# Optimization experiments

Measured on AMD Instinct MI355X. Metric: run time of the kernel, lower is better.

## Reference

```python
import jax, jax.numpy as jnp
import numpy as np

B, L, CIN, C = 256, 65, 2053, 512
SCALE = 1.0 / float(np.sqrt(C))


def _attn_layer(x, Wq, bq, Wk, bk, Wv, bv):
    # x: [B, Cin, L]; Conv1d(kernel=1) == channel-mixing matmul
    q = jnp.einsum('oi,bil->bol', Wq, x) + bq[:, None]
    k = jnp.einsum('oi,bil->bol', Wk, x) + bk[:, None]
    v = jax.nn.leaky_relu(jnp.einsum('oi,bil->bol', Wv, x) + bv[:, None], 0.01)
    # att[b,l,m] = <q[:,l], k[:,m]> / sqrt(C); softmax over m
    att = jax.nn.softmax(jnp.einsum('bcl,bcm->blm', q, k) * SCALE, axis=-1)
    # original: sum_m att[b,l,1,m] * v[b,1,c,m] -> [B,L,C] -> permute -> [B,C,L]
    out = jnp.einsum('blm,bcm->bcl', att, v)
    return out + x if out.shape == x.shape else out  # residual only when channels match


def _transform(x, Wq0, bq0, Wk0, bk0, Wv0, bv0, Wq, bq, Wk, bk, Wv, bv):
    x = _attn_layer(x, Wq0, bq0, Wk0, bk0, Wv0, bv0)
    for n in range(3):  # layers 1..3, C->C with residual
        x = _attn_layer(x, Wq[n], bq[n], Wk[n], bk[n], Wv[n], bv[n])
    return x


def setup_inputs():
    key = jax.random.key(0)
    ks = jax.random.split(key, 20)
    s = 0.02
    inp = {
        'dataleft': jax.random.normal(ks[0], (B, L, CIN), jnp.float32),
        'dataright': jax.random.normal(ks[1], (B, L, CIN), jnp.float32),
        # layer-0 QKV conv1d (k=1) weights: [C, CIN]
        'Wq0': jax.random.normal(ks[2], (C, CIN), jnp.float32) * s,
        'bq0': jnp.zeros((C,), jnp.float32),
        'Wk0': jax.random.normal(ks[3], (C, CIN), jnp.float32) * s,
        'bk0': jnp.zeros((C,), jnp.float32),
        'Wv0': jax.random.normal(ks[4], (C, CIN), jnp.float32) * s,
        'bv0': jnp.zeros((C,), jnp.float32),
        # layers 1..3 stacked: [3, C, C]
        'Wq': jax.random.normal(ks[5], (3, C, C), jnp.float32) * s,
        'bq': jnp.zeros((3, C), jnp.float32),
        'Wk': jax.random.normal(ks[6], (3, C, C), jnp.float32) * s,
        'bk': jnp.zeros((3, C), jnp.float32),
        'Wv': jax.random.normal(ks[7], (3, C, C), jnp.float32) * s,
        'bv': jnp.zeros((3, C), jnp.float32),
        # classifier: fc1(1024->256), fc2(256->2)
        'W1': jax.random.normal(ks[8], (256, 2 * C), jnp.float32) * s,
        'b1': jnp.zeros((256,), jnp.float32),
        'W2': jax.random.normal(ks[9], (2, 256), jnp.float32) * s,
        'b2': jnp.zeros((2,), jnp.float32),
    }
    return inp


def reference(dataleft, dataright, Wq0, bq0, Wk0, bk0, Wv0, bv0,
              Wq, bq, Wk, bk, Wv, bv, W1, b1, W2, b2):
    xl = jnp.transpose(dataleft, (0, 2, 1))   # [B, CIN, L]
    xr = jnp.transpose(dataright, (0, 2, 1))
    xl = _transform(xl, Wq0, bq0, Wk0, bk0, Wv0, bv0, Wq, bq, Wk, bk, Wv, bv)
    xr = _transform(xr, Wq0, bq0, Wk0, bk0, Wv0, bv0, Wq, bq, Wk, bk, Wv, bv)
    # AdaptiveAvgPool2d((512,1)) on [B,512,L]: identity over channel dim, mean over L
    xl = jnp.mean(xl, axis=-1)  # [B, C]
    xr = jnp.mean(xr, axis=-1)
    h = jnp.concatenate([xl, xr], axis=1)            # [B, 2C]
    h = jax.nn.relu(h @ W1.T + b1)                   # [B, 256]
    y = h @ W2.T + b2                                # [B, 2]
    return y  # training mode: no final softmax
```

## Files before the change

### kernel.cpp

```cpp
#include <hip/hip_runtime.h>
#include <hip/hip_bf16.h>

#define BF16 __hip_bfloat16

typedef __bf16 bf16x8 __attribute__((ext_vector_type(8)));
typedef float f32x4 __attribute__((ext_vector_type(4)));

__device__ __forceinline__ void async_copy16(const void* g, void* l) {
    __builtin_amdgcn_global_load_lds(
        (const __attribute__((address_space(1))) void*)g,
        (__attribute__((address_space(3))) void*)l,
        16, 0, 0);
}

__global__ __launch_bounds__(256) void convert_pad_k(
    const float* __restrict__ src, BF16* __restrict__ dst,
    int Ks, int Kd) {
    const long r = blockIdx.y;
    const int k = (blockIdx.x * 256 + threadIdx.x) * 2;
    if (k >= Kd) return;
    float a = (k < Ks) ? src[r * Ks + k] : 0.f;
    float b = (k + 1 < Ks) ? src[r * Ks + k + 1] : 0.f;
    dst[r * Kd + k] = __float2bfloat16(a);
    dst[r * Kd + k + 1] = __float2bfloat16(b);
}

__global__ __launch_bounds__(512, 2) void gemm_qkv(
    const BF16* __restrict__ Xg, const BF16* __restrict__ Wg,
    const float* __restrict__ bqp, const float* __restrict__ bkp, const float* __restrict__ bvp,
    BF16* __restrict__ Qo, BF16* __restrict__ Ko, BF16* __restrict__ Vo,
    int K) {
    __shared__ __align__(16) BF16 As[3][256 * 64];
    __shared__ __align__(16) BF16 Bs[3][128 * 64];
    const int tid = threadIdx.x;
    const int w = tid >> 6;
    const int lane = tid & 63;
    const int quad = lane >> 4;
    const int l15 = lane & 15;
    const int linear = blockIdx.x + 12 * blockIdx.y;
    const int cpx = (12 * (int)gridDim.y) >> 3;
    const int id2 = (linear & 7) * cpx + (linear >> 3);
    const int bx = id2 % 12;
    const int by = id2 / 12;
    const long n0 = (long)by * 256;
    const long m0full = (long)bx * 128;
    const int sel = bx >> 2;
    const int mbase = (bx & 3) * 128;
    const int wr = (w >> 1) * 64;
    const int wc = (w & 1) * 64;
    const int KT = K >> 6;
    const int rl = lane >> 3;
    const int gsw = ((lane & 7) ^ (rl & 7)) * 8;
    const int rw = w * 8 + rl;

#define STAGE_TILE(k0, buf)                                                              \
    do {                                                                                 \
        _Pragma("unroll")                                                                \
        for (int r_ = 0; r_ < 4; ++r_)                                                   \
            async_copy16(Xg + (n0 + r_ * 64 + rw) * K + (k0) + gsw,                      \
                         &As[buf][(r_ * 64 + w * 8) * 64]);                              \
        _Pragma("unroll")                                                                \
        for (int r_ = 0; r_ < 2; ++r_)                                                   \
            async_copy16(Wg + (m0full + r_ * 64 + rw) * K + (k0) + gsw,                  \
                         &Bs[buf][(r_ * 64 + w * 8) * 64]);                              \
    } while (0)

    f32x4 acc[4][4] = {};
    STAGE_TILE(0, 0);
    STAGE_TILE(64, 1);
    int cb = 0;
    for (int kt = 0; kt < KT; ++kt) {
        if (kt + 1 < KT) {
            asm volatile("s_waitcnt vmcnt(6)\n\ts_barrier" ::: "memory");
        } else {
            asm volatile("s_waitcnt vmcnt(0)\n\ts_barrier" ::: "memory");
        }
        __builtin_amdgcn_sched_barrier(0);
        bf16x8 af[2][4], bfr[2][4];
#pragma unroll
        for (int s = 0; s < 2; ++s) {
#pragma unroll
            for (int i = 0; i < 4; ++i) {
                const int row = wr + i * 16 + l15;
                const int gx = ((s * 4 + quad) ^ (row & 7)) * 8;
                af[s][i] = *(const bf16x8*)&As[cb][row * 64 + gx];
            }
#pragma unroll
            for (int j = 0; j < 4; ++j) {
                const int row = wc + j * 16 + l15;
                const int gx = ((s * 4 + quad) ^ (row & 7)) * 8;
                bfr[s][j] = *(const bf16x8*)&Bs[cb][row * 64 + gx];
            }
        }
        if (kt + 2 < KT) {
            int nb = cb + 2;
            if (nb >= 3) nb -= 3;
            STAGE_TILE((kt + 2) << 6, nb);
        }
        __builtin_amdgcn_s_setprio(1);
#pragma unroll
        for (int s = 0; s < 2; ++s)
#pragma unroll
            for (int i = 0; i < 4; ++i)
#pragma unroll
                for (int j = 0; j < 4; ++j)
                    acc[i][j] = __builtin_amdgcn_mfma_f32_16x16x32_bf16(af[s][i], bfr[s][j], acc[i][j], 0, 0, 0);
        __builtin_amdgcn_s_setprio(0);
        ++cb;
        if (cb >= 3) cb -= 3;
    }
#undef STAGE_TILE

    const float* bp = (sel == 0) ? bqp : (sel == 1) ? bkp : bvp;
    BF16* out = (sel == 0) ? Qo : (sel == 1) ? Ko : Vo;
#pragma unroll
    for (int j = 0; j < 4; ++j) {
        const int m = mbase + wc + j * 16 + l15;
        const float bz = bp[m];
#pragma unroll
        for (int i = 0; i < 4; ++i) {
#pragma unroll
            for (int r = 0; r < 4; ++r) {
                const long n = n0 + wr + i * 16 + quad * 4 + r;
                float v = acc[i][j][r] + bz;
                if (sel == 2) v = (v >= 0.f) ? v : 0.01f * v;
                out[n * 512 + m] = __float2bfloat16(v);
            }
        }
    }
}

__global__ __launch_bounds__(256) void vtrans_k(const ushort* __restrict__ Vb,
                                                ushort* __restrict__ Vt) {
    const int bb = blockIdx.x;
    for (int idx = threadIdx.x; idx < 512 * 48; idx += 256) {
        const int c = idx / 48;
        const int m = (idx - c * 48) * 2;
        ushort a = (m < 65) ? Vb[((long)bb * 65 + m) * 512 + c] : (ushort)0;
        ushort b = (m + 1 < 65) ? Vb[((long)bb * 65 + m + 1) * 512 + c] : (ushort)0;
        *(uint*)&Vt[((long)bb * 512 + c) * 96 + m] = (uint)a | ((uint)b << 16);
    }
}

__global__ __launch_bounds__(256) void attn_scores(
    const BF16* __restrict__ Qg, const BF16* __restrict__ Kg, BF16* __restrict__ Pg) {
    constexpr float SC = 0.04419417382415922f;
    __shared__ __align__(16) BF16 Qs[2][80 * 32];
    __shared__ __align__(16) BF16 Ks[2][80 * 32];
    __shared__ float Sf[80 * 84];
    const int bb = blockIdx.x;
    const int tid = threadIdx.x;
    const int w = tid >> 6, lane = tid & 63, quad = lane >> 4, l15 = lane & 15;
    int i16a[7], j16a[7];
#pragma unroll
    for (int u = 0; u < 7; ++u) {
        const int t = w + 4 * u;
        const int tc = (t < 25) ? t : 0;
        i16a[u] = (tc / 5) * 16;
        j16a[u] = (tc % 5) * 16;
    }
    f32x4 acc[7] = {};
    for (int k0 = 0; k0 < 512; k0 += 64) {
        for (int idx = tid; idx < 1280; idx += 256) {
            const int t = (idx >= 640) ? 1 : 0;
            const int e = idx - t * 640;
            const int sub = (e >= 320) ? 1 : 0;
            const int e2 = e - sub * 320;
            const int row = e2 >> 2;
            const int koff = (e2 & 3) * 8;
            uint4 val = make_uint4(0, 0, 0, 0);
            if (row < 65) {
                const BF16* src = (t ? Kg : Qg) + ((long)(bb * 65 + row) * 512 + k0 + sub * 32 + koff);
                val = *(const uint4*)src;
            }
            *(uint4*)&((t ? Ks : Qs)[sub][row * 32 + koff]) = val;
        }
        __syncthreads();
#pragma unroll
        for (int sub = 0; sub < 2; ++sub) {
#pragma unroll
            for (int u = 0; u < 7; ++u) {
                if (w + 4 * u < 25) {
                    bf16x8 af = *(const bf16x8*)&Qs[sub][(i16a[u] + l15) * 32 + quad * 8];
                    bf16x8 bfr = *(const bf16x8*)&Ks[sub][(j16a[u] + l15) * 32 + quad * 8];
                    acc[u] = __builtin_amdgcn_mfma_f32_16x16x32_bf16(af, bfr, acc[u], 0, 0, 0);
                }
            }
        }
        __syncthreads();
    }
#pragma unroll
    for (int u = 0; u < 7; ++u) {
        if (w + 4 * u < 25) {
#pragma unroll
            for (int r = 0; r < 4; ++r)
                Sf[(i16a[u] + quad * 4 + r) * 84 + j16a[u] + l15] = acc[u][r] * SC;
        }
    }
    __syncthreads();
    for (int rr = tid >> 2; rr < 65; rr += 64) {
        const int sub = tid & 3;
        float mx = -1e30f;
        for (int m = sub; m < 65; m += 4) mx = fmaxf(mx, Sf[rr * 84 + m]);
        mx = fmaxf(mx, __shfl_xor(mx, 1));
        mx = fmaxf(mx, __shfl_xor(mx, 2));
        float s = 0.f;
        for (int m = sub; m < 65; m += 4) {
            float e = __expf(Sf[rr * 84 + m] - mx);
            Sf[rr * 84 + m] = e;
            s += e;
        }
        s += __shfl_xor(s, 1);
        s += __shfl_xor(s, 2);
        const float inv = 1.f / s;
        const long base = ((long)bb * 65 + rr) * 96;
        for (int m = sub; m < 96; m += 4) {
            float v = (m < 65) ? Sf[rr * 84 + m] * inv : 0.f;
            Pg[base + m] = __float2bfloat16(v);
        }
    }
}

__global__ __launch_bounds__(256) void attn_pv(
    const BF16* __restrict__ Pg, const BF16* __restrict__ Vt,
    BF16* __restrict__ Xg, int residual) {
    __shared__ __align__(16) BF16 Ps[80 * 104];
    const int bb = blockIdx.x;
    const int c0 = blockIdx.y * 128;
    const int tid = threadIdx.x;
    const int w = tid >> 6, lane = tid & 63, quad = lane >> 4, l15 = lane & 15;
    for (int idx = tid; idx < 960; idx += 256) {
        const int row = idx / 12;
        const int kk = idx - row * 12;
        uint4 val = make_uint4(0, 0, 0, 0);
        if (row < 65) val = *(const uint4*)(Pg + ((long)bb * 65 + row) * 96 + kk * 8);
        *(uint4*)&Ps[row * 104 + kk * 8] = val;
    }
    __syncthreads();
    bf16x8 af[5][3];
#pragma unroll
    for (int i = 0; i < 5; ++i)
#pragma unroll
        for (int ks = 0; ks < 3; ++ks)
            af[i][ks] = *(const bf16x8*)&Ps[(i * 16 + l15) * 104 + ks * 32 + quad * 8];
#pragma unroll
    for (int jj = 0; jj < 2; ++jj) {
        const int c = c0 + (jj * 4 + w) * 16 + l15;
        const BF16* vp = Vt + ((long)bb * 512 + c) * 96 + quad * 8;
        bf16x8 b0 = *(const bf16x8*)vp;
        bf16x8 b1 = *(const bf16x8*)(vp + 32);
        bf16x8 b2 = *(const bf16x8*)(vp + 64);
        f32x4 po[5] = {};
#pragma unroll
        for (int i = 0; i < 5; ++i) {
            po[i] = __builtin_amdgcn_mfma_f32_16x16x32_bf16(af[i][0], b0, po[i], 0, 0, 0);
            po[i] = __builtin_amdgcn_mfma_f32_16x16x32_bf16(af[i][1], b1, po[i], 0, 0, 0);
            po[i] = __builtin_amdgcn_mfma_f32_16x16x32_bf16(af[i][2], b2, po[i], 0, 0, 0);
        }
#pragma unroll
        for (int i = 0; i < 5; ++i)
#pragma unroll
            for (int r = 0; r < 4; ++r) {
                const int l = i * 16 + quad * 4 + r;
                if (l < 65) {
                    const long idx = ((long)(bb * 65 + l)) * 512 + c;
                    float v = po[i][r];
                    if (residual) v += __bfloat162float(Xg[idx]);
                    Xg[idx] = __float2bfloat16(v);
                }
            }
    }
}

__global__ __launch_bounds__(256) void pool_k(const BF16* __restrict__ Xg,
                                              float* __restrict__ Hp) {
    const int sb = blockIdx.x;
    const int s = sb >> 8, b = sb & 255;
    for (int c = threadIdx.x; c < 512; c += 256) {
        float acc = 0.f;
        for (int l = 0; l < 65; ++l)
            acc += __bfloat162float(Xg[((long)sb * 65 + l) * 512 + c]);
        Hp[(long)b * 1024 + s * 512 + c] = acc * (1.f / 65.f);
    }
}

__global__ __launch_bounds__(256) void fc_k(
    const float* __restrict__ Hp, const float* __restrict__ W1,
    const float* __restrict__ b1, const float* __restrict__ W2,
    const float* __restrict__ b2, float* __restrict__ out) {
    __shared__ float h[1024];
    __shared__ float h1[256];
    const int b = blockIdx.x, tid = threadIdx.x;
    for (int k = tid; k < 1024; k += 256) h[k] = Hp[(long)b * 1024 + k];
    __syncthreads();
    float acc = b1[tid];
    for (int k = 0; k < 1024; ++k) acc += W1[(long)tid * 1024 + k] * h[k];
    h1[tid] = fmaxf(acc, 0.f);
    __syncthreads();
    const int w = tid >> 6, lane = tid & 63;
    if (w < 2) {
        float p = 0.f;
        for (int u = lane; u < 256; u += 64) p += W2[w * 256 + u] * h1[u];
        for (int off = 32; off > 0; off >>= 1) p += __shfl_down(p, off);
        if (lane == 0) out[b * 2 + w] = p + b2[w];
    }
}

extern "C" void kernel_launch(void* const* d_in, const int* in_sizes, int n_in,
                              void* d_out, int out_size, void* d_ws, size_t ws_size,
                              hipStream_t stream) {
    const float* dataL = (const float*)d_in[0];
    const float* dataR = (const float*)d_in[1];
    const float* Wq0 = (const float*)d_in[2];
    const float* bq0 = (const float*)d_in[3];
    const float* Wk0 = (const float*)d_in[4];
    const float* bk0 = (const float*)d_in[5];
    const float* Wv0 = (const float*)d_in[6];
    const float* bv0 = (const float*)d_in[7];
    const float* Wq = (const float*)d_in[8];
    const float* bq = (const float*)d_in[9];
    const float* Wk = (const float*)d_in[10];
    const float* bk = (const float*)d_in[11];
    const float* Wv = (const float*)d_in[12];
    const float* bv = (const float*)d_in[13];
    const float* W1 = (const float*)d_in[14];
    const float* b1 = (const float*)d_in[15];
    const float* W2 = (const float*)d_in[16];
    const float* b2 = (const float*)d_in[17];

    char* ws = (char*)d_ws;
    BF16* Xb = (BF16*)ws;
    BF16* X = Xb;
    BF16* Vt = (BF16*)(ws + 34078720L);
    BF16* Pg = (BF16*)(ws + 84410368L);
    float* Hp = (float*)(ws + 90800128L);
    BF16* Wc = (BF16*)(ws + 140574720L);
    BF16* Qb = (BF16*)(ws + 151781376L);
    BF16* Kb = (BF16*)(ws + 185860096L);
    BF16* Vb = (BF16*)(ws + 219938816L);

    BF16* w0 = Wc;
    BF16* wl = Wc + 3L * 512 * 2112;

    auto cvt = [&](const float* src, BF16* dst, long R, int Ks, int Kd) {
        dim3 grid((Kd / 2 + 255) / 256, (unsigned)R);
        convert_pad_k<<<grid, 256, 0, stream>>>(src, dst, Ks, Kd);
    };
    cvt(dataL, Xb, 16640, 2053, 2112);
    cvt(dataR, Xb + 16640L * 2112, 16640, 2053, 2112);
    cvt(Wq0, w0, 512, 2053, 2112);
    cvt(Wk0, w0 + 512L * 2112, 512, 2053, 2112);
    cvt(Wv0, w0 + 2L * 512 * 2112, 512, 2053, 2112);
    for (int n = 0; n < 3; ++n) {
        BF16* base = wl + (long)n * 3 * 262144;
        cvt(Wq + (long)n * 262144, base, 512, 512, 512);
        cvt(Wk + (long)n * 262144, base + 262144, 512, 512, 512);
        cvt(Wv + (long)n * 262144, base + 2 * 262144, 512, 512, 512);
    }

    dim3 ggrid(12, 130);
    dim3 pvgrid(512, 4);
    gemm_qkv<<<ggrid, 512, 0, stream>>>(Xb, w0, bq0, bk0, bv0, Qb, Kb, Vb, 2112);
    vtrans_k<<<512, 256, 0, stream>>>((const ushort*)Vb, (ushort*)Vt);
    attn_scores<<<512, 256, 0, stream>>>(Qb, Kb, Pg);
    attn_pv<<<pvgrid, 256, 0, stream>>>(Pg, Vt, X, 0);
    for (int n = 0; n < 3; ++n) {
        gemm_qkv<<<ggrid, 512, 0, stream>>>(X, wl + (long)n * 3 * 262144,
                                            bq + n * 512, bk + n * 512, bv + n * 512,
                                            Qb, Kb, Vb, 512);
        vtrans_k<<<512, 256, 0, stream>>>((const ushort*)Vb, (ushort*)Vt);
        attn_scores<<<512, 256, 0, stream>>>(Qb, Kb, Pg);
        attn_pv<<<pvgrid, 256, 0, stream>>>(Pg, Vt, X, 1);
    }
    pool_k<<<512, 256, 0, stream>>>(X, Hp);
    fc_k<<<256, 256, 0, stream>>>(Hp, W1, b1, W2, b2, (float*)d_out);
}
```

Measured before the change: 1.308 ms.

## Fuse V transpose, attention scores, softmax and PV into one kernel

```diff
diff --git a/kernel.cpp b/kernel.cpp
--- a/kernel.cpp
+++ b/kernel.cpp
@@ -17,19 +17,24 @@
     const float* __restrict__ src, BF16* __restrict__ dst,
     int Ks, int Kd) {
     const long r = blockIdx.y;
-    const int k = (blockIdx.x * 256 + threadIdx.x) * 2;
+    const int k = (blockIdx.x * 256 + threadIdx.x) * 4;
     if (k >= Kd) return;
-    float a = (k < Ks) ? src[r * Ks + k] : 0.f;
-    float b = (k + 1 < Ks) ? src[r * Ks + k + 1] : 0.f;
-    dst[r * Kd + k] = __float2bfloat16(a);
-    dst[r * Kd + k + 1] = __float2bfloat16(b);
-}
-
+    const float* s = src + r * (long)Ks;
+    float a0 = (k < Ks) ? s[k] : 0.f;
+    float a1 = (k + 1 < Ks) ? s[k + 1] : 0.f;
+    float a2 = (k + 2 < Ks) ? s[k + 2] : 0.f;
+    float a3 = (k + 3 < Ks) ? s[k + 3] : 0.f;
+    BF16 b0 = __float2bfloat16(a0), b1 = __float2bfloat16(a1);
+    BF16 b2 = __float2bfloat16(a2), b3 = __float2bfloat16(a3);
+    ushort4 o = make_ushort4(*(ushort*)&b0, *(ushort*)&b1, *(ushort*)&b2, *(ushort*)&b3);
+    *(ushort4*)&dst[r * (long)Kd + k] = o;
+}
+
+template <int K>
 __global__ __launch_bounds__(512, 2) void gemm_qkv(
     const BF16* __restrict__ Xg, const BF16* __restrict__ Wg,
     const float* __restrict__ bqp, const float* __restrict__ bkp, const float* __restrict__ bvp,
-    BF16* __restrict__ Qo, BF16* __restrict__ Ko, BF16* __restrict__ Vo,
-    int K) {
+    BF16* __restrict__ Qo, BF16* __restrict__ Ko, BF16* __restrict__ Vo) {
     __shared__ __align__(16) BF16 As[3][256 * 64];
     __shared__ __align__(16) BF16 Bs[3][128 * 64];
     const int tid = threadIdx.x;
@@ -48,7 +53,7 @@
     const int mbase = (bx & 3) * 128;
     const int wr = (w >> 1) * 64;
     const int wc = (w & 1) * 64;
-    const int KT = K >> 6;
+    constexpr int KT = K >> 6;
     const int rl = lane >> 3;
     const int gsw = ((lane & 7) ^ (rl & 7)) * 8;
     const int rw = w * 8 + rl;
@@ -130,27 +135,19 @@
     }
 }
 
-__global__ __launch_bounds__(256) void vtrans_k(const ushort* __restrict__ Vb,
-                                                ushort* __restrict__ Vt) {
-    const int bb = blockIdx.x;
-    for (int idx = threadIdx.x; idx < 512 * 48; idx += 256) {
-        const int c = idx / 48;
-        const int m = (idx - c * 48) * 2;
-        ushort a = (m < 65) ? Vb[((long)bb * 65 + m) * 512 + c] : (ushort)0;
-        ushort b = (m + 1 < 65) ? Vb[((long)bb * 65 + m + 1) * 512 + c] : (ushort)0;
-        *(uint*)&Vt[((long)bb * 512 + c) * 96 + m] = (uint)a | ((uint)b << 16);
-    }
-}
-
-__global__ __launch_bounds__(256) void attn_scores(
-    const BF16* __restrict__ Qg, const BF16* __restrict__ Kg, BF16* __restrict__ Pg) {
+__global__ __launch_bounds__(256) void attn_fused(
+    const BF16* __restrict__ Qg, const BF16* __restrict__ Kg, const BF16* __restrict__ Vg,
+    BF16* __restrict__ Xg, int residual) {
     constexpr float SC = 0.04419417382415922f;
-    __shared__ __align__(16) BF16 Qs[2][80 * 32];
-    __shared__ __align__(16) BF16 Ks[2][80 * 32];
+    __shared__ __align__(16) char Us[26624];
     __shared__ float Sf[80 * 84];
+    __shared__ __align__(16) BF16 Pl[80 * 104];
+    BF16* qk = (BF16*)Us;
+    BF16* Vtl = (BF16*)Us;
     const int bb = blockIdx.x;
     const int tid = threadIdx.x;
     const int w = tid >> 6, lane = tid & 63, quad = lane >> 4, l15 = lane & 15;
+
     int i16a[7], j16a[7];
 #pragma unroll
     for (int u = 0; u < 7; ++u) {
@@ -173,7 +170,7 @@
                 const BF16* src = (t ? Kg : Qg) + ((long)(bb * 65 + row) * 512 + k0 + sub * 32 + koff);
                 val = *(const uint4*)src;
             }
-            *(uint4*)&((t ? Ks : Qs)[sub][row * 32 + koff]) = val;
+            *(uint4*)&qk[(t * 2 + sub) * 2560 + row * 32 + koff] = val;
         }
         __syncthreads();
 #pragma unroll
@@ -181,8 +178,8 @@
 #pragma unroll
             for (int u = 0; u < 7; ++u) {
                 if (w + 4 * u < 25) {
-                    bf16x8 af = *(const bf16x8*)&Qs[sub][(i16a[u] + l15) * 32 + quad * 8];
-                    bf16x8 bfr = *(const bf16x8*)&Ks[sub][(j16a[u] + l15) * 32 + quad * 8];
+                    bf16x8 af = *(const bf16x8*)&qk[sub * 2560 + (i16a[u] + l15) * 32 + quad * 8];
+                    bf16x8 bfr = *(const bf16x8*)&qk[(2 + sub) * 2560 + (j16a[u] + l15) * 32 + quad * 8];
                     acc[u] = __builtin_amdgcn_mfma_f32_16x16x32_bf16(af, bfr, acc[u], 0, 0, 0);
                 }
             }
@@ -213,62 +210,69 @@
         s += __shfl_xor(s, 1);
         s += __shfl_xor(s, 2);
         const float inv = 1.f / s;
-        const long base = ((long)bb * 65 + rr) * 96;
         for (int m = sub; m < 96; m += 4) {
             float v = (m < 65) ? Sf[rr * 84 + m] * inv : 0.f;
-            Pg[base + m] = __float2bfloat16(v);
-        }
-    }
-}
-
-__global__ __launch_bounds__(256) void attn_pv(
-    const BF16* __restrict__ Pg, const BF16* __restrict__ Vt,
-    BF16* __restrict__ Xg, int residual) {
-    __shared__ __align__(16) BF16 Ps[80 * 104];
-    const int bb = blockIdx.x;
-    const int c0 = blockIdx.y * 128;
-    const int tid = threadIdx.x;
-    const int w = tid >> 6, lane = tid & 63, quad = lane >> 4, l15 = lane & 15;
-    for (int idx = tid; idx < 960; idx += 256) {
-        const int row = idx / 12;
-        const int kk = idx - row * 12;
-        uint4 val = make_uint4(0, 0, 0, 0);
-        if (row < 65) val = *(const uint4*)(Pg + ((long)bb * 65 + row) * 96 + kk * 8);
-        *(uint4*)&Ps[row * 104 + kk * 8] = val;
+            Pl[rr * 104 + m] = __float2bfloat16(v);
+        }
+    }
+    for (int idx = tid; idx < 15 * 48; idx += 256) {
+        const int row = 65 + idx / 48;
+        const int col = (idx - (idx / 48) * 48) * 2;
+        *(uint*)&Pl[row * 104 + col] = 0u;
+    }
+    for (int idx = tid; idx < 128 * 32; idx += 256) {
+        const int m = 65 + (idx & 31);
+        if (m < 96) Vtl[(idx >> 5) * 104 + m] = (BF16)0.f;
     }
     __syncthreads();
+
     bf16x8 af[5][3];
 #pragma unroll
     for (int i = 0; i < 5; ++i)
 #pragma unroll
         for (int ks = 0; ks < 3; ++ks)
-            af[i][ks] = *(const bf16x8*)&Ps[(i * 16 + l15) * 104 + ks * 32 + quad * 8];
-#pragma unroll
-    for (int jj = 0; jj < 2; ++jj) {
-        const int c = c0 + (jj * 4 + w) * 16 + l15;
-        const BF16* vp = Vt + ((long)bb * 512 + c) * 96 + quad * 8;
-        bf16x8 b0 = *(const bf16x8*)vp;
-        bf16x8 b1 = *(const bf16x8*)(vp + 32);
-        bf16x8 b2 = *(const bf16x8*)(vp + 64);
-        f32x4 po[5] = {};
-#pragma unroll
-        for (int i = 0; i < 5; ++i) {
-            po[i] = __builtin_amdgcn_mfma_f32_16x16x32_bf16(af[i][0], b0, po[i], 0, 0, 0);
-            po[i] = __builtin_amdgcn_mfma_f32_16x16x32_bf16(af[i][1], b1, po[i], 0, 0, 0);
-            po[i] = __builtin_amdgcn_mfma_f32_16x16x32_bf16(af[i][2], b2, po[i], 0, 0, 0);
-        }
-#pragma unroll
-        for (int i = 0; i < 5; ++i)
-#pragma unroll
-            for (int r = 0; r < 4; ++r) {
-                const int l = i * 16 + quad * 4 + r;
-                if (l < 65) {
-                    const long idx = ((long)(bb * 65 + l)) * 512 + c;
-                    float v = po[i][r];
-                    if (residual) v += __bfloat162float(Xg[idx]);
-                    Xg[idx] = __float2bfloat16(v);
+            af[i][ks] = *(const bf16x8*)&Pl[(i * 16 + l15) * 104 + ks * 32 + quad * 8];
+
+    for (int cc = 0; cc < 4; ++cc) {
+        const int c0 = cc * 128;
+        for (int idx = tid; idx < 65 * 16; idx += 256) {
+            const int m = idx >> 4;
+            const int cg = idx & 15;
+            uint4 val = *(const uint4*)(Vg + ((long)(bb * 65 + m) * 512 + c0 + cg * 8));
+            const ushort* u = (const ushort*)&val;
+#pragma unroll
+            for (int j = 0; j < 8; ++j)
+                *(ushort*)&Vtl[(cg * 8 + j) * 104 + m] = u[j];
+        }
+        __syncthreads();
+#pragma unroll
+        for (int jj = 0; jj < 2; ++jj) {
+            const int ch = (jj * 4 + w) * 16 + l15;
+            const int c = c0 + ch;
+            bf16x8 b0 = *(const bf16x8*)&Vtl[ch * 104 + quad * 8];
+            bf16x8 b1 = *(const bf16x8*)&Vtl[ch * 104 + 32 + quad * 8];
+            bf16x8 b2 = *(const bf16x8*)&Vtl[ch * 104 + 64 + quad * 8];
+            f32x4 po[5] = {};
+#pragma unroll
+            for (int i = 0; i < 5; ++i) {
+                po[i] = __builtin_amdgcn_mfma_f32_16x16x32_bf16(af[i][0], b0, po[i], 0, 0, 0);
+                po[i] = __builtin_amdgcn_mfma_f32_16x16x32_bf16(af[i][1], b1, po[i], 0, 0, 0);
+                po[i] = __builtin_amdgcn_mfma_f32_16x16x32_bf16(af[i][2], b2, po[i], 0, 0, 0);
+            }
+#pragma unroll
+            for (int i = 0; i < 5; ++i)
+#pragma unroll
+                for (int r = 0; r < 4; ++r) {
+                    const int l = i * 16 + quad * 4 + r;
+                    if (l < 65) {
+                        const long idx = ((long)(bb * 65 + l)) * 512 + c;
+                        float v = po[i][r];
+                        if (residual) v += __bfloat162float(Xg[idx]);
+                        Xg[idx] = __float2bfloat16(v);
+                    }
                 }
-            }
+        }
+        __syncthreads();
     }
 }
 
@@ -331,8 +335,6 @@
     char* ws = (char*)d_ws;
     BF16* Xb = (BF16*)ws;
     BF16* X = Xb;
-    BF16* Vt = (BF16*)(ws + 34078720L);
-    BF16* Pg = (BF16*)(ws + 84410368L);
     float* Hp = (float*)(ws + 90800128L);
     BF16* Wc = (BF16*)(ws + 140574720L);
     BF16* Qb = (BF16*)(ws + 151781376L);
@@ -343,7 +345,7 @@
     BF16* wl = Wc + 3L * 512 * 2112;
 
     auto cvt = [&](const float* src, BF16* dst, long R, int Ks, int Kd) {
-        dim3 grid((Kd / 2 + 255) / 256, (unsigned)R);
+        dim3 grid((Kd / 4 + 255) / 256, (unsigned)R);
         convert_pad_k<<<grid, 256, 0, stream>>>(src, dst, Ks, Kd);
     };
     cvt(dataL, Xb, 16640, 2053, 2112);
@@ -359,18 +361,13 @@
     }
 
     dim3 ggrid(12, 130);
-    dim3 pvgrid(512, 4);
-    gemm_qkv<<<ggrid, 512, 0, stream>>>(Xb, w0, bq0, bk0, bv0, Qb, Kb, Vb, 2112);
-    vtrans_k<<<512, 256, 0, stream>>>((const ushort*)Vb, (ushort*)Vt);
-    attn_scores<<<512, 256, 0, stream>>>(Qb, Kb, Pg);
-    attn_pv<<<pvgrid, 256, 0, stream>>>(Pg, Vt, X, 0);
+    gemm_qkv<2112><<<ggrid, 512, 0, stream>>>(Xb, w0, bq0, bk0, bv0, Qb, Kb, Vb);
+    attn_fused<<<512, 256, 0, stream>>>(Qb, Kb, Vb, X, 0);
     for (int n = 0; n < 3; ++n) {
-        gemm_qkv<<<ggrid, 512, 0, stream>>>(X, wl + (long)n * 3 * 262144,
-                                            bq + n * 512, bk + n * 512, bv + n * 512,
-                                            Qb, Kb, Vb, 512);
-        vtrans_k<<<512, 256, 0, stream>>>((const ushort*)Vb, (ushort*)Vt);
-        attn_scores<<<512, 256, 0, stream>>>(Qb, Kb, Pg);
-        attn_pv<<<pvgrid, 256, 0, stream>>>(Pg, Vt, X, 1);
+        gemm_qkv<512><<<ggrid, 512, 0, stream>>>(X, wl + (long)n * 3 * 262144,
+                                                 bq + n * 512, bk + n * 512, bv + n * 512,
+                                                 Qb, Kb, Vb);
+        attn_fused<<<512, 256, 0, stream>>>(Qb, Kb, Vb, X, 1);
     }
     pool_k<<<512, 256, 0, stream>>>(X, Hp);
     fc_k<<<256, 256, 0, stream>>>(Hp, W1, b1, W2, b2, (float*)d_out);
```

New measurement: 1.166 ms. -10.8%, faster.
